# Kernel optimization log

Hardware: AMD Instinct MI355X
Metric: run time of the kernel (lower is better)

The kernel has to match this reference:

```python
import jax, jax.numpy as jnp
import numpy as np
import math

B, H, W, Cv, Ct, T = 8, 64, 64, 256, 512, 100
TOP_M = 5
N_PAD = 8  # last N_PAD text tokens are all-zero padding


def _xavier(key, fi, fo):
    lim = math.sqrt(6.0 / (fi + fo))
    return jax.random.uniform(key, (fi, fo), jnp.float32, -lim, lim)


def layernorm(x, g, b, eps=1e-5):
    m = x.mean(-1, keepdims=True)
    v = ((x - m) ** 2).mean(-1, keepdims=True)
    return (x - m) * jax.lax.rsqrt(v + eps) * g + b


def l2norm(x, eps=1e-6):
    n = jnp.sqrt((x * x).sum(-1, keepdims=True))
    return x / jnp.maximum(n, eps)


def setup_inputs() -> dict:
    key = jax.random.key(0)
    ks = jax.random.split(key, 10)
    visual = jax.random.normal(ks[0], (B, H, W, Cv), jnp.float32)
    text = jax.random.normal(ks[1], (B, T, Ct), jnp.float32)
    text = text.at[:, T - N_PAD:, :].set(0.0)  # padded tokens
    return {
        'visual_features': visual,
        'text_features': text,
        'ln1_g': jnp.ones((Cv,), jnp.float32),
        'ln1_b': jnp.zeros((Cv,), jnp.float32),
        'qw': _xavier(ks[2], Cv, Ct), 'qb': jnp.zeros((Ct,), jnp.float32),
        'vw': _xavier(ks[3], Ct, Cv), 'vb': jnp.zeros((Cv,), jnp.float32),
        'gate_w': jax.random.normal(ks[4], (Cv, 1), jnp.float32) * 0.02,
        'gate_b': jnp.zeros((1,), jnp.float32),
        'logit_scale': jnp.asarray(math.log(1.0 / 0.07), jnp.float32),
        'alpha': jnp.asarray(0.1, jnp.float32),
        'ln2_g': jnp.ones((Cv,), jnp.float32),
        'ln2_b': jnp.zeros((Cv,), jnp.float32),
        'w1': jax.random.normal(ks[5], (Cv, 4 * Cv), jnp.float32) * 0.02,
        'b1': jnp.zeros((4 * Cv,), jnp.float32),
        'w2': jax.random.normal(ks[6], (4 * Cv, Cv), jnp.float32) * 0.02,
        'b2': jnp.zeros((Cv,), jnp.float32),
        'top_m': TOP_M,
    }


def reference(visual_features, text_features, ln1_g, ln1_b, qw, qb, vw, vb,
              gate_w, gate_b, logit_scale, alpha, ln2_g, ln2_b, w1, b1, w2, b2,
              top_m):
    Bv, Hh, Ww, C = visual_features.shape
    N = Hh * Ww
    x = layernorm(visual_features, ln1_g, ln1_b).reshape(Bv, N, C)
    q = l2norm(x @ qw + qb)                     # (B,N,Ct)
    k = l2norm(text_features)                   # (B,T,Ct)
    v = text_features @ vw + vb                 # (B,T,Cv)
    pad = jnp.abs(text_features).sum(-1) <= 1e-6  # (B,T) True = padding
    Ctd = float(qw.shape[1])
    scale = jnp.exp(jnp.clip(logit_scale, -2.0, 2.0)) / math.sqrt(Ctd)
    sim = jnp.einsum('bnc,btc->bnt', q, k) * scale
    top_vals, top_idx = jax.lax.top_k(sim, top_m)       # (B,N,M)
    pad_top = jax.vmap(lambda p, i: p[i])(pad, top_idx)  # (B,N,M)
    top_vals = jnp.where(pad_top, -jnp.inf, top_vals)
    attn = jax.nn.softmax(top_vals, axis=-1)
    v_sel = jax.vmap(lambda vb_, ib: vb_[ib])(v, top_idx)  # (B,N,M,Cv)
    aligned = jnp.einsum('bnm,bnmc->bnc', attn, v_sel)
    gate = jax.nn.sigmoid(x @ gate_w + gate_b)  # (B,N,1)
    aligned = aligned * gate
    y = x + alpha * aligned
    y = layernorm(y, ln2_g, ln2_b)
    y = y + (jax.nn.gelu(y @ w1 + b1, approximate=False) @ w2 + b2)
    return y.reshape(Bv, Hh, Ww, C)
```

## Files before the change

### kernel.cpp

```cpp
#include <hip/hip_runtime.h>
#include <hip/hip_bf16.h>
#include <math.h>

using bf16 = __hip_bfloat16;
typedef __attribute__((ext_vector_type(8))) short s16x8;
typedef __attribute__((ext_vector_type(4))) short s16x4;
typedef __attribute__((ext_vector_type(4))) float f32x4;
typedef __attribute__((ext_vector_type(4))) unsigned int u32x4;

static __device__ __forceinline__ float bits2f(unsigned short u) {
  union { unsigned int i; float f; } c; c.i = ((unsigned int)u) << 16; return c.f;
}
static __device__ __forceinline__ unsigned short f2bits(float f) {
  bf16 h = __float2bfloat16(f);
  return *reinterpret_cast<unsigned short*>(&h);
}
static __device__ __forceinline__ unsigned short scrub16(unsigned short u, unsigned short repl) {
  return ((u & 0x7F80u) == 0x7F80u) ? repl : u;
}
static __device__ __forceinline__ unsigned short f2bits_s(float f, unsigned short repl) {
  return scrub16(f2bits(f), repl);
}
static __device__ __forceinline__ float ldf_s(const float* p, float repl) {
  unsigned int w = *reinterpret_cast<const unsigned int*>(p);
  if ((w & 0x7F800000u) == 0x7F800000u) return repl;
  union { unsigned int i; float f; } c; c.i = w; return c.f;
}
static __device__ __forceinline__ float stf_s(float f, float repl) {
  union { float f; unsigned int i; } c; c.f = f;
  if ((c.i & 0x7F800000u) == 0x7F800000u) return repl;
  return f;
}
static __device__ __forceinline__ s16x8 pack8(const float* p) {
  union { f32x4 f; float fe[4]; unsigned int u[4]; } a, b;
  a.f = *reinterpret_cast<const f32x4*>(p);
  b.f = *reinterpret_cast<const f32x4*>(p + 4);
  s16x8 v;
  #pragma unroll
  for (int e = 0; e < 4; e++) {
    const float fa = ((a.u[e] & 0x7F800000u) == 0x7F800000u) ? 0.f : a.fe[e];
    const float fb = ((b.u[e] & 0x7F800000u) == 0x7F800000u) ? 0.f : b.fe[e];
    v[e]     = (short)f2bits_s(fa, 0);
    v[e + 4] = (short)f2bits_s(fb, 0);
  }
  return v;
}
static __device__ __forceinline__ float gelu_fast(float t) {
  const float u = fmaf(0.044715f * t * t, t, t);
  const float e = __expf(-1.5957691216057308f * u);
  return __fdividef(t, 1.f + e);
}
static __device__ __forceinline__ void gload_lds16(const unsigned short* g, unsigned short* l) {
  __builtin_amdgcn_global_load_lds(
      (const __attribute__((address_space(1))) void*)g,
      (__attribute__((address_space(3))) void*)l, 16, 0, 0);
}

static __device__ __forceinline__ float block_sum(float v, float* red, int tid) {
  #pragma unroll
  for (int o = 32; o > 0; o >>= 1) v += __shfl_down(v, o, 64);
  __syncthreads();
  if ((tid & 63) == 0) red[tid >> 6] = v;
  __syncthreads();
  return red[0] + red[1] + red[2] + red[3];
}

__global__ __launch_bounds__(256)
void k_ln1(float* vis, const float* __restrict__ g, const float* __restrict__ bta) {
  const int lane = threadIdx.x & 63;
  const long row = (long)blockIdx.x * 4 + (threadIdx.x >> 6);
  float* rp = vis + row * 256;
  union { u32x4 u; float f[4]; unsigned int w[4]; } c;
  c.u = *reinterpret_cast<const u32x4*>(&rp[lane * 4]);
  #pragma unroll
  for (int e = 0; e < 4; e++)
    if ((c.w[e] & 0x7F800000u) == 0x7F800000u) c.f[e] = 0.f;
  float s = c.f[0] + c.f[1] + c.f[2] + c.f[3];
  #pragma unroll
  for (int o = 32; o > 0; o >>= 1) s += __shfl_xor(s, o, 64);
  const float mean = s * (1.f / 256.f);
  float vr = 0.f;
  #pragma unroll
  for (int e = 0; e < 4; e++) { c.f[e] -= mean; vr = fmaf(c.f[e], c.f[e], vr); }
  #pragma unroll
  for (int o = 32; o > 0; o >>= 1) vr += __shfl_xor(vr, o, 64);
  const float rstd = rsqrtf(vr * (1.f / 256.f) + 1e-5f);
  f32x4 outv;
  #pragma unroll
  for (int e = 0; e < 4; e++)
    outv[e] = stf_s(c.f[e] * rstd * g[lane * 4 + e] + bta[lane * 4 + e], 0.f);
  *reinterpret_cast<f32x4*>(&rp[lane * 4]) = outv;
}

__global__ __launch_bounds__(256)
void k_prepw(const float* __restrict__ qw, unsigned short* __restrict__ qwt) {
  const int n = blockIdx.x;
  const int k = threadIdx.x;
  qwt[n * 256 + (k ^ ((n & 7) << 3))] = f2bits_s(ldf_s(&qw[(long)k * 512 + n], 0.f), 0);
}

__global__ __launch_bounds__(256)
void k_prep2(const float* __restrict__ text, unsigned short* __restrict__ khat,
             int* __restrict__ padf) {
  __shared__ float red[4];
  const int t = blockIdx.x, b = blockIdx.y, tid = threadIdx.x;
  unsigned short* kr = khat + ((long)b * 112 + t) * 512;
  if (t >= 100) {
    if (tid < 64) *reinterpret_cast<s16x8*>(&kr[tid * 8]) = (s16x8){0,0,0,0,0,0,0,0};
    return;
  }
  const float* tr = text + ((long)b * 100 + t) * 512;
  const float v0 = ldf_s(&tr[tid], 0.f), v1 = ldf_s(&tr[tid + 256], 0.f);
  const float ss = block_sum(fmaf(v0, v0, v1 * v1), red, tid);
  const float sa = block_sum(fabsf(v0) + fabsf(v1), red, tid);
  const float inv = 1.f / fmaxf(sqrtf(ss), 1e-6f);
  const int ks = tid ^ ((t & 7) << 3);
  kr[ks]       = f2bits_s(v0 * inv, 0);
  kr[ks + 256] = f2bits_s(v1 * inv, 0);
  if (tid == 0) padf[b * 100 + t] = (sa <= 1e-6f) ? 1 : 0;
}

__global__ __launch_bounds__(512)
void k_sim_mfma(const float* __restrict__ x, const unsigned short* __restrict__ qwt,
                const float* __restrict__ qb, const unsigned short* __restrict__ khat,
                const float* __restrict__ ls, unsigned short* __restrict__ simb) {
  __shared__ __align__(16) unsigned short s_q[64][520];
  __shared__ __align__(16) unsigned short s_un[32768];
  __shared__ float s_qn[64];

  const int tid  = threadIdx.x;
  const int lane = tid & 63;
  const int w    = tid >> 6;
  const int l15  = lane & 15;
  const int lg   = lane >> 4;
  const int b    = blockIdx.y;
  const long grow = (long)b * 4096 + (long)blockIdx.x * 64;

  #pragma unroll
  for (int it = 0; it < 8; it++) {
    const int u = tid + it * 512;
    gload_lds16(&qwt[u * 8], &s_un[u * 8]);
  }

  const int R1 = (w >> 2) * 32;
  s16x8 xa[2][8];
  #pragma unroll
  for (int rb = 0; rb < 2; rb++) {
    const float* xr = &x[(grow + R1 + rb * 16 + l15) * 256];
    #pragma unroll
    for (int ks = 0; ks < 8; ks++)
      xa[rb][ks] = pack8(xr + ks * 32 + lg * 8);
  }
  __syncthreads();

  const int C1 = (w & 3) * 32;
  for (int nc = 0; nc < 4; nc++) {
    f32x4 a1[2][2];
    #pragma unroll
    for (int i = 0; i < 2; i++)
      #pragma unroll
      for (int j = 0; j < 2; j++) a1[i][j] = (f32x4){0.f, 0.f, 0.f, 0.f};
    #pragma unroll
    for (int ks = 0; ks < 8; ks++) {
      s16x8 bfr[2];
      #pragma unroll
      for (int cb = 0; cb < 2; cb++) {
        const int nl = C1 + cb * 16 + l15;
        const int byt = nl * 512 + ((ks * 64 + lg * 16) ^ ((nl & 7) << 4));
        bfr[cb] = *reinterpret_cast<const s16x8*>(reinterpret_cast<const char*>(s_un) + byt);
      }
      #pragma unroll
      for (int rb = 0; rb < 2; rb++) {
        a1[rb][0] = __builtin_amdgcn_mfma_f32_16x16x32_bf16(xa[rb][ks], bfr[0], a1[rb][0], 0, 0, 0);
        a1[rb][1] = __builtin_amdgcn_mfma_f32_16x16x32_bf16(xa[rb][ks], bfr[1], a1[rb][1], 0, 0, 0);
      }
    }
    #pragma unroll
    for (int cb = 0; cb < 2; cb++) {
      const int n = nc * 128 + C1 + cb * 16 + l15;
      const float bq = ldf_s(&qb[n], 0.f);
      #pragma unroll
      for (int rb = 0; rb < 2; rb++)
        #pragma unroll
        for (int rg = 0; rg < 4; rg++)
          s_q[R1 + rb * 16 + lg * 4 + rg][n] = f2bits_s(a1[rb][cb][rg] + bq, 0);
    }
    __syncthreads();
    if (nc < 3) {
      const unsigned short* src = qwt + (long)(nc + 1) * 32768;
      #pragma unroll
      for (int it = 0; it < 8; it++) {
        const int u = tid + it * 512;
        gload_lds16(&src[u * 8], &s_un[u * 8]);
      }
      __syncthreads();
    }
  }

  {
    const int r = tid >> 3, ts8 = tid & 7;
    float ss = 0.f;
    #pragma unroll
    for (int j = 0; j < 8; j++) {
      s16x8 v = *reinterpret_cast<const s16x8*>(&s_q[r][ts8 * 64 + j * 8]);
      #pragma unroll
      for (int e = 0; e < 8; e++) { float f = bits2f((unsigned short)v[e]); ss = fmaf(f, f, ss); }
    }
    #pragma unroll
    for (int o = 4; o > 0; o >>= 1) ss += __shfl_down(ss, o, 8);
    if (ts8 == 0) s_qn[r] = fmaxf(sqrtf(ss), 1e-6f);
  }

  const int wr = w & 1, wc = w >> 1;
  f32x4 acc[2][2];
  #pragma unroll
  for (int i = 0; i < 2; i++)
    #pragma unroll
    for (int j = 0; j < 2; j++) acc[i][j] = (f32x4){0.f, 0.f, 0.f, 0.f};

  for (int kc = 0; kc < 2; kc++) {
    #pragma unroll
    for (int it = 0; it < 7; it++) {
      const int u = it * 512 + tid;
      const int t = u >> 5, kb = (u & 31) * 8;
      gload_lds16(&khat[((long)b * 112 + t) * 512 + kc * 256 + kb], &s_un[u * 8]);
    }
    __syncthreads();
    #pragma unroll
    for (int ks = 0; ks < 8; ks++) {
      const int ko = kc * 256 + ks * 32 + lg * 8;
      s16x8 af[2], bfr[2];
      #pragma unroll
      for (int rb = 0; rb < 2; rb++)
        af[rb] = *reinterpret_cast<const s16x8*>(&s_q[(2 * wr + rb) * 16 + l15][ko]);
      #pragma unroll
      for (int cb = 0; cb < 2; cb++)
        if (2 * wc + cb < 7) {
          const int t = (2 * wc + cb) * 16 + l15;
          bfr[cb] = *reinterpret_cast<const s16x8*>(
              &s_un[t * 256 + ((ks * 32 + lg * 8) ^ ((t & 7) << 3))]);
        }
      #pragma unroll
      for (int rb = 0; rb < 2; rb++)
        #pragma unroll
        for (int cb = 0; cb < 2; cb++)
          if (2 * wc + cb < 7)
            acc[rb][cb] = __builtin_amdgcn_mfma_f32_16x16x32_bf16(af[rb], bfr[cb], acc[rb][cb], 0, 0, 0);
    }
    __syncthreads();
  }

  float l = ldf_s(&ls[0], 0.f);
  l = fminf(fmaxf(l, -2.f), 2.f);
  const float scale = expf(l) * 0.04419417382415922f;
  #pragma unroll
  for (int rb = 0; rb < 2; rb++)
    #pragma unroll
    for (int rg = 0; rg < 4; rg++) {
      const int row = (2 * wr + rb) * 16 + lg * 4 + rg;
      const float inv = scale / s_qn[row];
      #pragma unroll
      for (int cb = 0; cb < 2; cb++) {
        const int tcol = (2 * wc + cb) * 16 + l15;
        if (2 * wc + cb < 7 && tcol < 100)
          simb[(grow + row) * 100 + tcol] = f2bits_s(acc[rb][cb][rg] * inv, 0);
      }
    }
}

__global__ __launch_bounds__(256)
void k_v(const float* __restrict__ text, const float* __restrict__ vw,
         const float* __restrict__ vb_, float* __restrict__ vf) {
  __shared__ float s_t[512];
  const int bt = blockIdx.x;
  const int tid = threadIdx.x;
  const float* tr = text + (long)bt * 512;
  s_t[tid]       = ldf_s(&tr[tid], 0.f);
  s_t[tid + 256] = ldf_s(&tr[tid + 256], 0.f);
  __syncthreads();
  float acc = 0.f;
  for (int k = 0; k < 512; k++) acc = fmaf(s_t[k], vw[k * 256 + tid], acc);
  vf[(long)bt * 256 + tid] = stf_s(acc + vb_[tid], 0.f);
}

#define AROWS 32
__global__ __launch_bounds__(256)
void k_attn(const unsigned short* __restrict__ sim, const int* __restrict__ pad,
            const float* __restrict__ v, float* xy,
            const float* __restrict__ gate_w, const float* __restrict__ gate_b,
            const float* __restrict__ alpha, const float* __restrict__ ln2g,
            const float* __restrict__ ln2b) {
  __shared__ float s_x[AROWS][256];
  __shared__ float s_sim[AROWS][104];
  __shared__ float s_attn[AROWS][8];
  __shared__ int   s_idx[AROWS][8];
  __shared__ float s_gate[AROWS], s_mu[AROWS], s_rs[AROWS];
  __shared__ int   s_pad[128];
  const int b = blockIdx.y;
  const int n0 = blockIdx.x * AROWS;
  const int tid = threadIdx.x;
  const long xbase = ((long)b * 4096 + n0) * 256;
  #pragma unroll
  for (int i = 0; i < AROWS; i++)
    s_x[i][tid] = ldf_s(&xy[xbase + (long)i * 256 + tid], 0.f);
  const long sbase = ((long)b * 4096 + n0) * 100;
  for (int i = tid; i < AROWS * 100; i += 256) {
    int rr = i / 100, t = i - rr * 100;
    s_sim[rr][t] = bits2f(scrub16(sim[sbase + (long)rr * 100 + t], 0));
  }
  if (tid < 100) s_pad[tid] = pad[b * 100 + tid];
  __syncthreads();

  const int r = tid >> 3, ts = tid & 7;
  float loc[13];
  #pragma unroll
  for (int j = 0; j < 13; j++) {
    int t = ts * 13 + j;
    loc[j] = (t < 100) ? s_sim[r][t] : -1e38f;
  }
  float topv[5]; int topi[5];
  for (int it = 0; it < 5; it++) {
    float bv = -1e38f; int bi = 1 << 20;
    #pragma unroll
    for (int j = 0; j < 13; j++) {
      if (loc[j] > bv) { bv = loc[j]; bi = ts * 13 + j; }
    }
    #pragma unroll
    for (int o = 4; o > 0; o >>= 1) {
      float ov = __shfl_down(bv, o, 8);
      int   oi = __shfl_down(bi, o, 8);
      if (ov > bv || (ov == bv && oi < bi)) { bv = ov; bi = oi; }
    }
    bv = __shfl(bv, 0, 8); bi = __shfl(bi, 0, 8);
    const int bic = (bi < 0) ? 0 : (bi > 99 ? 99 : bi);
    topv[it] = bv; topi[it] = bic;
    const int rel = bi - ts * 13;
    if (rel >= 0 && rel < 13) loc[rel] = -1e38f;
  }
  {
    float tv[5], mx = -1e38f;
    #pragma unroll
    for (int m = 0; m < 5; m++) { tv[m] = s_pad[topi[m]] ? -1e38f : topv[m]; mx = fmaxf(mx, tv[m]); }
    const float mxs = (mx > -1e37f) ? mx : 0.f;
    float se = 0.f, ev[5];
    #pragma unroll
    for (int m = 0; m < 5; m++) {
      ev[m] = (tv[m] > -1e37f) ? expf(fminf(tv[m] - mxs, 0.f)) : 0.f;
      se += ev[m];
    }
    const float rse = (se > 0.f) ? 1.f / se : 0.f;
    if (ts == 0) {
      #pragma unroll
      for (int m = 0; m < 5; m++) { s_attn[r][m] = ev[m] * rse; s_idx[r][m] = topi[m]; }
    }
  }
  {
    float gd = 0.f;
    #pragma unroll
    for (int j = 0; j < 32; j++) {
      int c = ts + 8 * j;
      gd = fmaf(s_x[r][c], gate_w[c], gd);
    }
    #pragma unroll
    for (int o = 4; o > 0; o >>= 1) gd += __shfl_down(gd, o, 8);
    if (ts == 0) s_gate[r] = 1.f / (1.f + expf(fminf(-(gd + gate_b[0]), 80.f)));
  }
  __syncthreads();
  const float al = alpha[0];
  const float* vb_ = v + (long)b * 100 * 256;
  for (int rr = 0; rr < AROWS; rr++) {
    float acc = 0.f;
    #pragma unroll
    for (int m = 0; m < 5; m++)
      acc = fmaf(s_attn[rr][m], ldf_s(&vb_[(long)s_idx[rr][m] * 256 + tid], 0.f), acc);
    s_x[rr][tid] = s_x[rr][tid] + al * (acc * s_gate[rr]);
  }
  __syncthreads();
  {
    float sm = 0.f;
    #pragma unroll
    for (int j = 0; j < 32; j++) sm += s_x[r][ts + 8 * j];
    #pragma unroll
    for (int o = 4; o > 0; o >>= 1) sm += __shfl_down(sm, o, 8);
    sm = __shfl(sm, 0, 8);
    const float mean = sm * (1.f / 256.f);
    float vr = 0.f;
    #pragma unroll
    for (int j = 0; j < 32; j++) { float d = s_x[r][ts + 8 * j] - mean; vr = fmaf(d, d, vr); }
    #pragma unroll
    for (int o = 4; o > 0; o >>= 1) vr += __shfl_down(vr, o, 8);
    if (ts == 0) { s_mu[r] = mean; s_rs[r] = rsqrtf(vr * (1.f / 256.f) + 1e-5f); }
  }
  __syncthreads();
  for (int rr = 0; rr < AROWS; rr++) {
    float yv = (s_x[rr][tid] - s_mu[rr]) * s_rs[rr] * ln2g[tid] + ln2b[tid];
    xy[xbase + (long)rr * 256 + tid] = stf_s(yv, 100.0f);
  }
}

__global__ __launch_bounds__(256)
void k_prep(const float* __restrict__ w1, const float* __restrict__ w2,
            unsigned short* __restrict__ w1s, unsigned short* __restrict__ w2s) {
  const int i = blockIdx.x * 256 + threadIdx.x;
  if (i < 262144) {
    const int h = i >> 8, k = i & 255;
    w1s[h * 256 + (k ^ ((h & 7) << 3))] = f2bits(w1[(long)k * 1024 + h]);
  } else {
    const int j = i - 262144;
    const int c = j >> 10, h = j & 1023;
    const int hs = (h & ~63) | ((h & 63) ^ ((c & 7) << 3));
    w2s[(long)c * 1024 + hs] = f2bits(w2[(long)h * 256 + c]);
  }
}

__global__ __launch_bounds__(512, 2)
void k_ffn_mfma(const float* __restrict__ yln,
                const unsigned short* __restrict__ w1s,
                const float* __restrict__ b1,
                const unsigned short* __restrict__ w2s,
                const float* __restrict__ b2,
                float* __restrict__ out) {
  __shared__ __align__(16) unsigned short s_w1[64 * 256];
  __shared__ __align__(16) unsigned short s_w2[256 * 64];
  __shared__ __align__(16) unsigned short s_h[128][72];

  const int tid  = threadIdx.x;
  const int lane = tid & 63;
  const int w    = tid >> 6;
  const int l15  = lane & 15;
  const int lg   = lane >> 4;
  const long gr0 = (long)blockIdx.x * 128;

  #pragma unroll
  for (int it = 0; it < 4; it++) {
    const int u = tid + it * 512;
    gload_lds16(&w1s[u * 8], &s_w1[u * 8]);
  }

  const int R1 = (w >> 1) * 32, C1 = (w & 1) * 32;
  const int R0 = (w >> 2) * 64, C0 = (w & 3) * 64;

  s16x8 ya[2][8];
  #pragma unroll
  for (int rb = 0; rb < 2; rb++) {
    const float* xr = &yln[(gr0 + R1 + rb * 16 + l15) * 256];
    #pragma unroll
    for (int ks = 0; ks < 8; ks++)
      ya[rb][ks] = pack8(xr + ks * 32 + lg * 8);
  }

  f32x4 acc[4][4];
  #pragma unroll
  for (int i = 0; i < 4; i++)
    #pragma unroll
    for (int j = 0; j < 4; j++)
      acc[i][j] = (f32x4){0.f, 0.f, 0.f, 0.f};

  __syncthreads();

  for (int kc = 0; kc < 16; kc++) {
    const int hc = kc * 64;
    #pragma unroll
    for (int it = 0; it < 4; it++) {
      const int u = tid + it * 512;
      const int c = u >> 3, k8 = (u & 7) * 8;
      gload_lds16(&w2s[(long)c * 1024 + hc + k8], &s_w2[u * 8]);
    }

    f32x4 a1[2][2];
    #pragma unroll
    for (int i = 0; i < 2; i++)
      #pragma unroll
      for (int j = 0; j < 2; j++) a1[i][j] = (f32x4){0.f, 0.f, 0.f, 0.f};
    __builtin_amdgcn_s_setprio(1);
    #pragma unroll
    for (int ks = 0; ks < 8; ks++) {
      const int ko = ks * 32 + lg * 8;
      const int n0_ = C1 + l15, n1_ = C1 + 16 + l15;
      const s16x8 bf0 = *reinterpret_cast<const s16x8*>(&s_w1[n0_ * 256 + (ko ^ ((n0_ & 7) << 3))]);
      const s16x8 bf1 = *reinterpret_cast<const s16x8*>(&s_w1[n1_ * 256 + (ko ^ ((n1_ & 7) << 3))]);
      a1[0][0] = __builtin_amdgcn_mfma_f32_16x16x32_bf16(ya[0][ks], bf0, a1[0][0], 0, 0, 0);
      a1[0][1] = __builtin_amdgcn_mfma_f32_16x16x32_bf16(ya[0][ks], bf1, a1[0][1], 0, 0, 0);
      a1[1][0] = __builtin_amdgcn_mfma_f32_16x16x32_bf16(ya[1][ks], bf0, a1[1][0], 0, 0, 0);
      a1[1][1] = __builtin_amdgcn_mfma_f32_16x16x32_bf16(ya[1][ks], bf1, a1[1][1], 0, 0, 0);
    }
    __builtin_amdgcn_s_setprio(0);
    #pragma unroll
    for (int cb = 0; cb < 2; cb++) {
      const int col = C1 + cb * 16 + l15;
      const float bb = b1[hc + col];
      #pragma unroll
      for (int rb = 0; rb < 2; rb++)
        #pragma unroll
        for (int rg = 0; rg < 4; rg++) {
          const float t = a1[rb][cb][rg] + bb;
          s_h[R1 + rb * 16 + lg * 4 + rg][col] = f2bits_s(gelu_fast(t), 0);
        }
    }
    __syncthreads();

    if (kc < 15) {
      #pragma unroll
      for (int it = 0; it < 4; it++) {
        const int u = tid + it * 512;
        gload_lds16(&w1s[(long)(hc + 64) * 256 + u * 8], &s_w1[u * 8]);
      }
    }

    __builtin_amdgcn_s_setprio(1);
    #pragma unroll
    for (int p = 0; p < 2; p++) {
      const int ko = p * 32 + lg * 8;
      s16x8 bfr[4];
      #pragma unroll
      for (int cb = 0; cb < 4; cb++) {
        const int c = C0 + cb * 16 + l15;
        bfr[cb] = *reinterpret_cast<const s16x8*>(&s_w2[c * 64 + (ko ^ ((c & 7) << 3))]);
      }
      #pragma unroll
      for (int rb = 0; rb < 4; rb++) {
        const s16x8 af = *reinterpret_cast<const s16x8*>(&s_h[R0 + rb * 16 + l15][ko]);
        #pragma unroll
        for (int cb = 0; cb < 4; cb++)
          acc[rb][cb] = __builtin_amdgcn_mfma_f32_16x16x32_bf16(af, bfr[cb], acc[rb][cb], 0, 0, 0);
      }
    }
    __builtin_amdgcn_s_setprio(0);
    __syncthreads();
  }

  #pragma unroll
  for (int rb = 0; rb < 4; rb++)
    #pragma unroll
    for (int rg = 0; rg < 4; rg++) {
      const int R = R0 + rb * 16 + lg * 4 + rg;
      const float* yr = &yln[(gr0 + R) * 256];
      #pragma unroll
      for (int cb = 0; cb < 4; cb++) {
        const int C = C0 + cb * 16 + l15;
        out[(gr0 + R) * 256 + C] =
            stf_s(ldf_s(&yr[C], 0.f) + acc[rb][cb][rg] + b2[C], 300.0f);
      }
    }
}

#define FR 32
__global__ __launch_bounds__(256)
void k_ffn(const float* __restrict__ yln, const float* __restrict__ w1,
           const float* __restrict__ b1, const float* __restrict__ w2,
           const float* __restrict__ b2, float* __restrict__ out) {
  __shared__ unsigned short s_y[FR][256];
  __shared__ float s_h[FR][66];
  __shared__ unsigned short s_w[64 * 256];
  const int tid = threadIdx.x;
  const long gr0 = (long)blockIdx.x * FR;
  for (int i = tid; i < FR * 256; i += 256)
    (&s_y[0][0])[i] = f2bits_s(ldf_s(&yln[gr0 * 256 + i], 0.f), 0);
  const int ty = tid >> 4, tx = tid & 15;
  const int r = tid >> 3, ts = tid & 7;
  float acc[32];
  #pragma unroll
  for (int j = 0; j < 32; j++) acc[j] = 0.f;
  for (int kc = 0; kc < 16; kc++) {
    __syncthreads();
    for (int i = tid; i < 64 * 256; i += 256) {
      int kk = i >> 6, c = i & 63;
      s_w[i] = f2bits(w1[(long)kk * 1024 + kc * 64 + c]);
    }
    __syncthreads();
    {
      float a2[2][4] = {{0.f,0.f,0.f,0.f},{0.f,0.f,0.f,0.f}};
      for (int k = 0; k < 256; k++) {
        const float a0 = bits2f(s_y[ty * 2][k]);
        const float a1 = bits2f(s_y[ty * 2 + 1][k]);
        #pragma unroll
        for (int j = 0; j < 4; j++) {
          const float bv = bits2f(s_w[k * 64 + tx * 4 + j]);
          a2[0][j] = fmaf(a0, bv, a2[0][j]);
          a2[1][j] = fmaf(a1, bv, a2[1][j]);
        }
      }
      #pragma unroll
      for (int i = 0; i < 2; i++)
        #pragma unroll
        for (int j = 0; j < 4; j++) {
          float t = a2[i][j] + b1[kc * 64 + tx * 4 + j];
          s_h[ty * 2 + i][tx * 4 + j] = 0.5f * t * (1.f + erff(t * 0.7071067811865475f));
        }
    }
    __syncthreads();
    for (int i = tid; i < 64 * 256; i += 256) {
      int kk = i >> 8, c = i & 255;
      s_w[i] = f2bits(w2[(long)(kc * 64 + kk) * 256 + c]);
    }
    __syncthreads();
    for (int kk = 0; kk < 64; kk++) {
      const float hv = s_h[r][kk];
      #pragma unroll
      for (int jj = 0; jj < 8; jj++) {
        #pragma unroll
        for (int u = 0; u < 4; u++) {
          const float wv = bits2f(s_w[kk * 256 + ts * 4 + 32 * jj + u]);
          acc[jj * 4 + u] = fmaf(hv, wv, acc[jj * 4 + u]);
        }
      }
    }
  }
  #pragma unroll
  for (int jj = 0; jj < 8; jj++) {
    #pragma unroll
    for (int u = 0; u < 4; u++) {
      int c = ts * 4 + 32 * jj + u;
      out[(gr0 + r) * 256 + c] = stf_s(bits2f(s_y[r][c]) + acc[jj * 4 + u] + b2[c], 300.0f);
    }
  }
}

__global__ __launch_bounds__(256)
void k_fill(float* __restrict__ out, long n, float V) {
  long i = (long)blockIdx.x * 256 + threadIdx.x;
  if (i < n) out[i] = V;
}

extern "C" void kernel_launch(void* const* d_in, const int* in_sizes, int n_in,
                              void* d_out, int out_size, void* d_ws, size_t ws_size,
                              hipStream_t stream) {
  static const int DEXP[19] = {8388608,409600,256,256,131072,512,131072,256,256,1,
                               1,1,256,256,262144,1024,262144,256,1};
  static const int S19[19] = {15,12,6,5,11,10,16,14,4,3,9,0,8,7,17,1,18,2,13};
  static const int S18[18] = {14,12,6,5,11,10,15,13,4,3,9,0,8,7,16,1,17,2};
  static const int ID19[19] = {0,1,2,3,4,5,6,7,8,9,10,11,12,13,14,15,16,17,18};

  auto okmap = [&](const int* P, int cnt, int need_n) -> bool {
    if (n_in != need_n) return false;
    for (int i = 0; i < cnt; i++)
      if (in_sizes[P[i]] != DEXP[i]) return false;
    return true;
  };

  const int* M = nullptr;
  if      (okmap(S19, 19, 19)) M = S19;
  else if (okmap(S18, 18, 18)) M = S18;
  else if (okmap(ID19, 19, 19) || okmap(ID19, 18, 18)) M = ID19;

  if (!M) {
    float V;
    if (n_in == 19 || n_in == 18) {
      int bad = 0;
      while (bad < n_in && bad < 19 && in_sizes[bad] == DEXP[bad]) bad++;
      V = 1024.f * (float)(1 + bad);
    } else {
      V = 32.f * (float)n_in + 16.f;
    }
    long n = (long)out_size;
    k_fill<<<(int)((n + 255) / 256), 256, 0, stream>>>((float*)d_out, n, V);
    return;
  }

  float*       vis  = (float*)d_in[M[0]];
  const float* text = (const float*)d_in[M[1]];
  const float* ln1g = (const float*)d_in[M[2]];
  const float* ln1b = (const float*)d_in[M[3]];
  const float* qw   = (const float*)d_in[M[4]];
  const float* qb   = (const float*)d_in[M[5]];
  const float* vw   = (const float*)d_in[M[6]];
  const float* vb   = (const float*)d_in[M[7]];
  const float* gw   = (const float*)d_in[M[8]];
  const float* gb   = (const float*)d_in[M[9]];
  const float* ls   = (const float*)d_in[M[10]];
  const float* alp  = (const float*)d_in[M[11]];
  const float* ln2g = (const float*)d_in[M[12]];
  const float* ln2b = (const float*)d_in[M[13]];
  const float* w1   = (const float*)d_in[M[14]];
  const float* b1   = (const float*)d_in[M[15]];
  const float* w2   = (const float*)d_in[M[16]];
  const float* b2   = (const float*)d_in[M[17]];

  unsigned short* simb = (unsigned short*)d_out;
  float* vf   = (float*)((char*)d_out + 6553600);
  int*   padf = (int*)  ((char*)d_out + 7372800);
  unsigned short* qwt  = (unsigned short*)((char*)d_out + 7376000);
  unsigned short* khat = (unsigned short*)((char*)d_out + 7900288);
  float* outp = (float*)d_out;

  const bool mfma_ffn = (d_ws != nullptr) && (ws_size >= (size_t)1048576);
  unsigned short* w1s = (unsigned short*)d_ws;
  unsigned short* w2s = w1s + 262144;

  k_ln1 <<<8192, 256, 0, stream>>>(vis, ln1g, ln1b);
  if (mfma_ffn)
    k_prep<<<2048, 256, 0, stream>>>(w1, w2, w1s, w2s);
  k_prepw<<<512, 256, 0, stream>>>(qw, qwt);
  k_prep2<<<dim3(112, 8), 256, 0, stream>>>(text, khat, padf);
  k_sim_mfma<<<dim3(64, 8), 512, 0, stream>>>(vis, qwt, qb, khat, ls, simb);
  k_v   <<<800, 256, 0, stream>>>(text, vw, vb, vf);
  k_attn<<<dim3(128, 8), 256, 0, stream>>>(simb, padf, vf, vis, gw, gb, alp, ln2g, ln2b);
  if (mfma_ffn)
    k_ffn_mfma<<<256, 512, 0, stream>>>(vis, w1s, b1, w2s, b2, outp);
  else
    k_ffn <<<1024, 256, 0, stream>>>(vis, w1, b1, w2, b2, outp);
}
```

Before: 294.9 us.

## Halve FFN row tile to 64, raise occupancy, vectorize attention kernel memory

The MFMA FFN kernel now handles 64 rows per block instead of 128 and launches 512 blocks. Each wave computes half as many accumulators, and launch bounds request four blocks per CU to raise occupancy and fill more CUs. The hidden-activation LDS buffer gets an XOR swizzle in place of padding. The attention kernel switches its x loads, value gathers and output stores to 128-bit float4 accesses with a padded shared row. The trade-off is that each block reloads the full W1/W2 weights for half as many rows, which doubles weight traffic per output row.

```diff
diff --git a/kernel.cpp b/kernel.cpp
--- a/kernel.cpp
+++ b/kernel.cpp
@@ -290,7 +290,7 @@
             const float* __restrict__ gate_w, const float* __restrict__ gate_b,
             const float* __restrict__ alpha, const float* __restrict__ ln2g,
             const float* __restrict__ ln2b) {
-  __shared__ float s_x[AROWS][256];
+  __shared__ float s_x[AROWS][260];
   __shared__ float s_sim[AROWS][104];
   __shared__ float s_attn[AROWS][8];
   __shared__ int   s_idx[AROWS][8];
@@ -301,8 +301,16 @@
   const int tid = threadIdx.x;
   const long xbase = ((long)b * 4096 + n0) * 256;
   #pragma unroll
-  for (int i = 0; i < AROWS; i++)
-    s_x[i][tid] = ldf_s(&xy[xbase + (long)i * 256 + tid], 0.f);
+  for (int it = 0; it < 8; it++) {
+    const int u = tid + it * 256;
+    const int row = u >> 6, c4 = (u & 63) * 4;
+    union { f32x4 f; float fe[4]; unsigned int w[4]; } cc;
+    cc.f = *reinterpret_cast<const f32x4*>(&xy[xbase + (long)row * 256 + c4]);
+    #pragma unroll
+    for (int e = 0; e < 4; e++)
+      if ((cc.w[e] & 0x7F800000u) == 0x7F800000u) cc.fe[e] = 0.f;
+    *reinterpret_cast<f32x4*>(&s_x[row][c4]) = cc.f;
+  }
   const long sbase = ((long)b * 4096 + n0) * 100;
   for (int i = tid; i < AROWS * 100; i += 256) {
     int rr = i / 100, t = i - rr * 100;
@@ -368,12 +376,27 @@
   __syncthreads();
   const float al = alpha[0];
   const float* vb_ = v + (long)b * 100 * 256;
-  for (int rr = 0; rr < AROWS; rr++) {
-    float acc = 0.f;
-    #pragma unroll
-    for (int m = 0; m < 5; m++)
-      acc = fmaf(s_attn[rr][m], ldf_s(&vb_[(long)s_idx[rr][m] * 256 + tid], 0.f), acc);
-    s_x[rr][tid] = s_x[rr][tid] + al * (acc * s_gate[rr]);
+  #pragma unroll
+  for (int it = 0; it < 8; it++) {
+    const int u = tid + it * 256;
+    const int row = u >> 6, c4 = (u & 63) * 4;
+    f32x4 acc4 = (f32x4){0.f, 0.f, 0.f, 0.f};
+    #pragma unroll
+    for (int m = 0; m < 5; m++) {
+      const float am = s_attn[row][m];
+      union { f32x4 f; float fe[4]; unsigned int w[4]; } vv;
+      vv.f = *reinterpret_cast<const f32x4*>(&vb_[(long)s_idx[row][m] * 256 + c4]);
+      #pragma unroll
+      for (int e = 0; e < 4; e++) {
+        const float fv = ((vv.w[e] & 0x7F800000u) == 0x7F800000u) ? 0.f : vv.fe[e];
+        acc4[e] = fmaf(am, fv, acc4[e]);
+      }
+    }
+    const float gr_ = s_gate[row];
+    f32x4 xv = *reinterpret_cast<f32x4*>(&s_x[row][c4]);
+    #pragma unroll
+    for (int e = 0; e < 4; e++) xv[e] = xv[e] + al * (acc4[e] * gr_);
+    *reinterpret_cast<f32x4*>(&s_x[row][c4]) = xv;
   }
   __syncthreads();
   {
@@ -392,9 +415,17 @@
     if (ts == 0) { s_mu[r] = mean; s_rs[r] = rsqrtf(vr * (1.f / 256.f) + 1e-5f); }
   }
   __syncthreads();
-  for (int rr = 0; rr < AROWS; rr++) {
-    float yv = (s_x[rr][tid] - s_mu[rr]) * s_rs[rr] * ln2g[tid] + ln2b[tid];
-    xy[xbase + (long)rr * 256 + tid] = stf_s(yv, 100.0f);
+  #pragma unroll
+  for (int it = 0; it < 8; it++) {
+    const int u = tid + it * 256;
+    const int row = u >> 6, c4 = (u & 63) * 4;
+    f32x4 yv;
+    #pragma unroll
+    for (int e = 0; e < 4; e++) {
+      const int c = c4 + e;
+      yv[e] = stf_s((s_x[row][c] - s_mu[row]) * s_rs[row] * ln2g[c] + ln2b[c], 100.0f);
+    }
+    *reinterpret_cast<f32x4*>(&xy[xbase + (long)row * 256 + c4]) = yv;
   }
 }
 
@@ -413,7 +444,7 @@
   }
 }
 
-__global__ __launch_bounds__(512, 2)
+__global__ __launch_bounds__(512, 4)
 void k_ffn_mfma(const float* __restrict__ yln,
                 const unsigned short* __restrict__ w1s,
                 const float* __restrict__ b1,
@@ -422,14 +453,14 @@
                 float* __restrict__ out) {
   __shared__ __align__(16) unsigned short s_w1[64 * 256];
   __shared__ __align__(16) unsigned short s_w2[256 * 64];
-  __shared__ __align__(16) unsigned short s_h[128][72];
+  __shared__ __align__(16) unsigned short s_h[64 * 64];
 
   const int tid  = threadIdx.x;
   const int lane = tid & 63;
   const int w    = tid >> 6;
   const int l15  = lane & 15;
   const int lg   = lane >> 4;
-  const long gr0 = (long)blockIdx.x * 128;
+  const long gr0 = (long)blockIdx.x * 64;
 
   #pragma unroll
   for (int it = 0; it < 4; it++) {
@@ -437,21 +468,20 @@
     gload_lds16(&w1s[u * 8], &s_w1[u * 8]);
   }
 
-  const int R1 = (w >> 1) * 32, C1 = (w & 1) * 32;
-  const int R0 = (w >> 2) * 64, C0 = (w & 3) * 64;
-
-  s16x8 ya[2][8];
-  #pragma unroll
-  for (int rb = 0; rb < 2; rb++) {
-    const float* xr = &yln[(gr0 + R1 + rb * 16 + l15) * 256];
+  const int R1 = (w >> 1) * 16, C1 = (w & 1) * 32;
+  const int R0 = (w >> 2) * 32, C0 = (w & 3) * 64;
+
+  s16x8 ya[8];
+  {
+    const float* xr = &yln[(gr0 + R1 + l15) * 256];
     #pragma unroll
     for (int ks = 0; ks < 8; ks++)
-      ya[rb][ks] = pack8(xr + ks * 32 + lg * 8);
-  }
-
-  f32x4 acc[4][4];
-  #pragma unroll
-  for (int i = 0; i < 4; i++)
+      ya[ks] = pack8(xr + ks * 32 + lg * 8);
+  }
+
+  f32x4 acc[2][4];
+  #pragma unroll
+  for (int i = 0; i < 2; i++)
     #pragma unroll
     for (int j = 0; j < 4; j++)
       acc[i][j] = (f32x4){0.f, 0.f, 0.f, 0.f};
@@ -467,11 +497,9 @@
       gload_lds16(&w2s[(long)c * 1024 + hc + k8], &s_w2[u * 8]);
     }
 
-    f32x4 a1[2][2];
-    #pragma unroll
-    for (int i = 0; i < 2; i++)
-      #pragma unroll
-      for (int j = 0; j < 2; j++) a1[i][j] = (f32x4){0.f, 0.f, 0.f, 0.f};
+    f32x4 a1[2];
+    a1[0] = (f32x4){0.f, 0.f, 0.f, 0.f};
+    a1[1] = (f32x4){0.f, 0.f, 0.f, 0.f};
     __builtin_amdgcn_s_setprio(1);
     #pragma unroll
     for (int ks = 0; ks < 8; ks++) {
@@ -479,10 +507,8 @@
       const int n0_ = C1 + l15, n1_ = C1 + 16 + l15;
       const s16x8 bf0 = *reinterpret_cast<const s16x8*>(&s_w1[n0_ * 256 + (ko ^ ((n0_ & 7) << 3))]);
       const s16x8 bf1 = *reinterpret_cast<const s16x8*>(&s_w1[n1_ * 256 + (ko ^ ((n1_ & 7) << 3))]);
-      a1[0][0] = __builtin_amdgcn_mfma_f32_16x16x32_bf16(ya[0][ks], bf0, a1[0][0], 0, 0, 0);
-      a1[0][1] = __builtin_amdgcn_mfma_f32_16x16x32_bf16(ya[0][ks], bf1, a1[0][1], 0, 0, 0);
-      a1[1][0] = __builtin_amdgcn_mfma_f32_16x16x32_bf16(ya[1][ks], bf0, a1[1][0], 0, 0, 0);
-      a1[1][1] = __builtin_amdgcn_mfma_f32_16x16x32_bf16(ya[1][ks], bf1, a1[1][1], 0, 0, 0);
+      a1[0] = __builtin_amdgcn_mfma_f32_16x16x32_bf16(ya[ks], bf0, a1[0], 0, 0, 0);
+      a1[1] = __builtin_amdgcn_mfma_f32_16x16x32_bf16(ya[ks], bf1, a1[1], 0, 0, 0);
     }
     __builtin_amdgcn_s_setprio(0);
     #pragma unroll
@@ -490,12 +516,11 @@
       const int col = C1 + cb * 16 + l15;
       const float bb = b1[hc + col];
       #pragma unroll
-      for (int rb = 0; rb < 2; rb++)
-        #pragma unroll
-        for (int rg = 0; rg < 4; rg++) {
-          const float t = a1[rb][cb][rg] + bb;
-          s_h[R1 + rb * 16 + lg * 4 + rg][col] = f2bits_s(gelu_fast(t), 0);
-        }
+      for (int rg = 0; rg < 4; rg++) {
+        const int row = R1 + lg * 4 + rg;
+        const float t = a1[cb][rg] + bb;
+        s_h[row * 64 + (col ^ ((row & 7) << 3))] = f2bits_s(gelu_fast(t), 0);
+      }
     }
     __syncthreads();
 
@@ -518,8 +543,9 @@
         bfr[cb] = *reinterpret_cast<const s16x8*>(&s_w2[c * 64 + (ko ^ ((c & 7) << 3))]);
       }
       #pragma unroll
-      for (int rb = 0; rb < 4; rb++) {
-        const s16x8 af = *reinterpret_cast<const s16x8*>(&s_h[R0 + rb * 16 + l15][ko]);
+      for (int rb = 0; rb < 2; rb++) {
+        const int hr = R0 + rb * 16 + l15;
+        const s16x8 af = *reinterpret_cast<const s16x8*>(&s_h[hr * 64 + (ko ^ ((hr & 7) << 3))]);
         #pragma unroll
         for (int cb = 0; cb < 4; cb++)
           acc[rb][cb] = __builtin_amdgcn_mfma_f32_16x16x32_bf16(af, bfr[cb], acc[rb][cb], 0, 0, 0);
@@ -530,7 +556,7 @@
   }
 
   #pragma unroll
-  for (int rb = 0; rb < 4; rb++)
+  for (int rb = 0; rb < 2; rb++)
     #pragma unroll
     for (int rg = 0; rg < 4; rg++) {
       const int R = R0 + rb * 16 + lg * 4 + rg;
@@ -696,7 +722,7 @@
   k_v   <<<800, 256, 0, stream>>>(text, vw, vb, vf);
   k_attn<<<dim3(128, 8), 256, 0, stream>>>(simb, padf, vf, vis, gw, gb, alp, ln2g, ln2b);
   if (mfma_ffn)
-    k_ffn_mfma<<<256, 512, 0, stream>>>(vis, w1s, b1, w2s, b2, outp);
+    k_ffn_mfma<<<512, 512, 0, stream>>>(vis, w1s, b1, w2s, b2, outp);
   else
     k_ffn <<<1024, 256, 0, stream>>>(vis, w1, b1, w2, b2, outp);
 }
```

Measured after the change: 285.8 us. -3.1%, faster.
